# Performance work log

Measured on AMD Instinct MI355X. Metric: run time of the kernel, lower is better.

Reference implementation:

```python
import jax, jax.numpy as jnp
import numpy as np

N_NODES = 131072       # 64 graphs * 2048 nodes
N_EDGES = 2097152      # avg degree 16
N_GRAPHS = 64
NODES_PER_GRAPH = 2048
D_IN = 128
D_EMB = 64
D_HID = 128
N_ACT = 2048


def setup_inputs() -> dict:
    key = jax.random.key(0)
    ks = jax.random.split(key, 12)
    s = lambda d: 1.0 / np.sqrt(d)
    return {
        "x": jax.random.normal(ks[0], (N_NODES, D_IN), dtype=jnp.float32),
        "edge_index": jax.random.randint(ks[1], (2, N_EDGES), 0, N_NODES, dtype=jnp.int32),
        "W1l": jax.random.normal(ks[2], (D_EMB, D_IN), dtype=jnp.float32) * s(D_IN),
        "b1l": jnp.zeros((D_EMB,), dtype=jnp.float32),
        "W1r": jax.random.normal(ks[3], (D_EMB, D_IN), dtype=jnp.float32) * s(D_IN),
        "W2l": jax.random.normal(ks[4], (D_EMB, D_EMB), dtype=jnp.float32) * s(D_EMB),
        "b2l": jnp.zeros((D_EMB,), dtype=jnp.float32),
        "W2r": jax.random.normal(ks[5], (D_EMB, D_EMB), dtype=jnp.float32) * s(D_EMB),
        "fc1_W": jax.random.normal(ks[6], (D_HID, D_EMB), dtype=jnp.float32) * s(D_EMB),
        "fc1_b": jnp.zeros((D_HID,), dtype=jnp.float32),
        "fc2_W": jax.random.normal(ks[7], (N_ACT, D_HID), dtype=jnp.float32) * s(D_HID),
        "fc2_b": jnp.zeros((N_ACT,), dtype=jnp.float32),
    }


def _sage_conv(x, src, dst, Wl, bl, Wr):
    # PyG SAGEConv (mean aggr): out = lin_l(mean_{j in N(i)} x_j) + lin_r(x_i)
    msg = x[src]                                              # [E, D] gather
    agg = jax.ops.segment_sum(msg, dst, num_segments=N_NODES)  # [N, D]
    cnt = jax.ops.segment_sum(jnp.ones((src.shape[0],), x.dtype), dst,
                              num_segments=N_NODES)
    mean = agg / jnp.maximum(cnt, 1.0)[:, None]
    return mean @ Wl.T + bl + x @ Wr.T


def reference(x, edge_index, W1l, b1l, W1r, W2l, b2l, W2r,
              fc1_W, fc1_b, fc2_W, fc2_b):
    src, dst = edge_index[0], edge_index[1]
    h1 = _sage_conv(x, src, dst, W1l, b1l, W1r)    # [N, D_EMB]
    h2 = _sage_conv(h1, src, dst, W2l, b2l, W2r)   # [N, D_EMB]
    g = h2.reshape(N_GRAPHS, NODES_PER_GRAPH, D_EMB).mean(axis=1)  # [B, D_EMB]
    h = jax.nn.relu(g @ fc1_W.T + fc1_b)
    q_values = h @ fc2_W.T + fc2_b                 # [B, N_ACT]
    return q_values
```

## Files before the change

kernel.cpp:

```cpp
#include <hip/hip_runtime.h>
#include <hip/hip_bf16.h>

#define D_IN 128
#define D_EMB 64

typedef float f32x2 __attribute__((ext_vector_type(2)));
typedef float f32x4v __attribute__((ext_vector_type(4)));
typedef short bf16x8 __attribute__((ext_vector_type(8)));

static __device__ __forceinline__ unsigned short f2bf(float f) {
  __hip_bfloat16 h = __float2bfloat16(f);
  return *(unsigned short*)&h;
}

__global__ __launch_bounds__(256) void wprep_mfma_k(const float* __restrict__ W,
                                                    unsigned short* __restrict__ out,
                                                    int K) {
  int tid = blockIdx.x * 256 + threadIdx.x;
  int total = (K / 32) * 4 * 64;
  if (tid >= total) return;
  int lane = tid & 63;
  int ct = (tid >> 6) & 3;
  int s = tid >> 8;
  int row = ct * 16 + (lane & 15);
  int kk = s * 32 + (lane >> 4) * 8;
  unsigned short tmp[8];
#pragma unroll
  for (int j = 0; j < 8; j++) tmp[j] = f2bf(W[row * K + kk + j]);
  *(uint4*)&out[(size_t)tid * 8] = *(uint4*)tmp;
}


__global__ __launch_bounds__(256) void bhist1_k(const int* __restrict__ key,
                                                int* __restrict__ bh, int E) {
  __shared__ int h[256];
  const int t = threadIdx.x;
  h[t] = 0;
  __syncthreads();
  const int base = blockIdx.x * 2048;
#pragma unroll
  for (int j = 0; j < 8; j++) {
    int e = base + j * 256 + t;
    if (e < E) atomicAdd(&h[key[e] >> 9], 1);
  }
  __syncthreads();
  bh[t * 1024 + blockIdx.x] = h[t];
}

__global__ __launch_bounds__(256) void scanA_k(int* __restrict__ bh,
                                               int* __restrict__ bintot) {
  __shared__ int sa[256], sb[256];
  const int t = threadIdx.x;
  int* row = bh + (size_t)blockIdx.x * 1024;
  int v0 = row[t * 4], v1 = row[t * 4 + 1], v2 = row[t * 4 + 2], v3 = row[t * 4 + 3];
  int sum = v0 + v1 + v2 + v3;
  sa[t] = sum;
  __syncthreads();
  int* in = sa;
  int* out = sb;
  for (int st = 1; st < 256; st <<= 1) {
    out[t] = in[t] + (t >= st ? in[t - st] : 0);
    __syncthreads();
    int* tmp = in; in = out; out = tmp;
  }
  int excl = in[t] - sum;
  row[t * 4] = excl;
  row[t * 4 + 1] = excl + v0;
  row[t * 4 + 2] = excl + v0 + v1;
  row[t * 4 + 3] = excl + v0 + v1 + v2;
  if (t == 255) bintot[blockIdx.x] = in[255];
}

__global__ __launch_bounds__(256) void scanB_k(const int* __restrict__ bintot,
                                               int* __restrict__ base) {
  __shared__ int sa[256], sb[256];
  const int t = threadIdx.x;
  int v = bintot[t];
  sa[t] = v;
  __syncthreads();
  int* in = sa;
  int* out = sb;
  for (int st = 1; st < 256; st <<= 1) {
    out[t] = in[t] + (t >= st ? in[t - st] : 0);
    __syncthreads();
    int* tmp = in; in = out; out = tmp;
  }
  base[t] = in[t] - v;
  if (t == 255) base[256] = in[255];
}

__global__ __launch_bounds__(256) void sfill_k(const int* __restrict__ src,
                                               const int* __restrict__ dst,
                                               const int* __restrict__ sh,
                                               const int* __restrict__ ssub,
                                               int* __restrict__ srcS,
                                               int* __restrict__ dstS, int E) {
  __shared__ int hA[256], hB[256], runCur[256], gb[256];
  __shared__ int scache[2048];
  __shared__ int dcache[2048];
  __shared__ int sortS[2048];
  __shared__ int sortD[2048];
  __shared__ unsigned short subb[2048];
  const int t = threadIdx.x;
  const int base = blockIdx.x * 2048;
  const int n = min(2048, E - base);
  hA[t] = 0;
  __syncthreads();
#pragma unroll
  for (int j = 0; j < 8; j++) {
    int idx = j * 256 + t;
    int e = base + idx;
    if (idx < n) {
      int s = src[e];
      scache[idx] = s;
      dcache[idx] = dst[e];
      atomicAdd(&hA[s >> 9], 1);
    }
  }
  __syncthreads();
  int cnt = hA[t];
  int* in = hA;
  int* out = hB;
  for (int st = 1; st < 256; st <<= 1) {
    out[t] = in[t] + (t >= st ? in[t - st] : 0);
    __syncthreads();
    int* tmp = in; in = out; out = tmp;
  }
  int rs = in[t] - cnt;
  __syncthreads();
  hB[t] = rs;
  runCur[t] = rs;
  gb[t] = ssub[t] + sh[t * 1024 + blockIdx.x];
  __syncthreads();
#pragma unroll
  for (int j = 0; j < 8; j++) {
    int idx = j * 256 + t;
    if (idx < n) {
      int s = scache[idx];
      int b = s >> 9;
      int lpos = atomicAdd(&runCur[b], 1);
      sortS[lpos] = s;
      sortD[lpos] = dcache[idx];
      subb[lpos] = (unsigned short)b;
    }
  }
  __syncthreads();
  for (int idx = t; idx < n; idx += 256) {
    int b = subb[idx];
    int g = gb[b] + idx - hB[b];
    srcS[g] = sortS[idx];
    dstS[g] = sortD[idx];
  }
}

__global__ __launch_bounds__(256) void bfill1_k(const int* __restrict__ src,
                                                const int* __restrict__ dst,
                                                const int* __restrict__ bh,
                                                const int* __restrict__ sbase,
                                                unsigned int* __restrict__ bkt,
                                                int E) {
  __shared__ int hA[256], hB[256], runCur[256], gb[256];
  __shared__ int dcache[2048];
  __shared__ unsigned int sorted[2048];
  __shared__ unsigned short subb[2048];
  const int t = threadIdx.x;
  const int base = blockIdx.x * 2048;
  const int n = min(2048, E - base);
  hA[t] = 0;
  __syncthreads();
#pragma unroll
  for (int j = 0; j < 8; j++) {
    int idx = j * 256 + t;
    int e = base + idx;
    if (idx < n) {
      int d = dst[e];
      dcache[idx] = d;
      atomicAdd(&hA[d >> 9], 1);
    }
  }
  __syncthreads();
  int cnt = hA[t];
  int* in = hA;
  int* out = hB;
  for (int st = 1; st < 256; st <<= 1) {
    out[t] = in[t] + (t >= st ? in[t - st] : 0);
    __syncthreads();
    int* tmp = in; in = out; out = tmp;
  }
  int rs = in[t] - cnt;
  __syncthreads();
  hB[t] = rs;
  runCur[t] = rs;
  gb[t] = sbase[t] + bh[t * 1024 + blockIdx.x];
  __syncthreads();
#pragma unroll
  for (int j = 0; j < 8; j++) {
    int idx = j * 256 + t;
    int e = base + idx;
    if (idx < n) {
      int d = dcache[idx];
      int b = d >> 9;
      int lpos = atomicAdd(&runCur[b], 1);
      sorted[lpos] = ((unsigned)(d & 511) << 17) | (unsigned)src[e];
      subb[lpos] = (unsigned short)b;
    }
  }
  __syncthreads();
  for (int idx = t; idx < n; idx += 256) {
    int b = subb[idx];
    bkt[gb[b] + idx - hB[b]] = sorted[idx];
  }
}

__global__ __launch_bounds__(256) void deg4_k(const unsigned int* __restrict__ bkt,
                                              const int* __restrict__ sbase,
                                              int* __restrict__ deg) {
  __shared__ int h[512];
  const int t = threadIdx.x;
  h[t] = 0;
  h[t + 256] = 0;
  __syncthreads();
  const int i = blockIdx.x;
  const int lo = sbase[i], hi = sbase[i + 1];
  for (int e = lo + t; e < hi; e += 256) atomicAdd(&h[bkt[e] >> 17], 1);
  __syncthreads();
  deg[i * 512 + t] = h[t];
  deg[i * 512 + t + 256] = h[t + 256];
}

__global__ __launch_bounds__(256) void blocksum_k(const int* __restrict__ deg,
                                                  int* __restrict__ bsum) {
  __shared__ int sm[256];
  int t = threadIdx.x;
  sm[t] = deg[blockIdx.x * 256 + t];
  __syncthreads();
  for (int s = 128; s > 0; s >>= 1) {
    if (t < s) sm[t] += sm[t + s];
    __syncthreads();
  }
  if (t == 0) bsum[blockIdx.x] = sm[0];
}

__global__ __launch_bounds__(256) void scanbsum_k(int* __restrict__ bsum) {
  __shared__ int a[512], b[512];
  int t = threadIdx.x;
  a[t] = bsum[t];
  a[t + 256] = bsum[t + 256];
  __syncthreads();
  int* in = a;
  int* out = b;
  for (int st = 1; st < 512; st <<= 1) {
    for (int i = t; i < 512; i += 256) out[i] = in[i] + (i >= st ? in[i - st] : 0);
    __syncthreads();
    int* tmp = in; in = out; out = tmp;
  }
  for (int i = t; i < 512; i += 256) bsum[i] = (i == 0) ? 0 : in[i - 1];
}

__global__ __launch_bounds__(256) void rowptr_k(const int* __restrict__ deg,
                                                const int* __restrict__ bsumEx,
                                                int* __restrict__ rowPtr,
                                                float* __restrict__ invdeg) {
  __shared__ int a[256], b[256];
  int t = threadIdx.x;
  int i = blockIdx.x * 256 + t;
  int d = deg[i];
  a[t] = d;
  __syncthreads();
  int* in = a;
  int* out = b;
  for (int st = 1; st < 256; st <<= 1) {
    out[t] = in[t] + (t >= st ? in[t - st] : 0);
    __syncthreads();
    int* tmp = in; in = out; out = tmp;
  }
  int incl = in[t] + bsumEx[blockIdx.x];
  rowPtr[i + 1] = incl;
  invdeg[i] = 1.0f / fmaxf((float)d, 1.0f);
  if (i == 0) rowPtr[0] = 0;
}

#define CSR_CAP 12032
__global__ __launch_bounds__(256) void scat4_k(const unsigned int* __restrict__ bkt,
                                               const int* __restrict__ sbase,
                                               const int* __restrict__ rowPtr,
                                               int* __restrict__ csr) {
  __shared__ int cur[512];
  __shared__ int cbuf[CSR_CAP];
  const int t = threadIdx.x;
  const int i = blockIdx.x;
  const int node0 = i * 512;
  const int base0 = rowPtr[node0];
  cur[t] = rowPtr[node0 + t] - base0;
  cur[t + 256] = rowPtr[node0 + t + 256] - base0;
  __syncthreads();
  const int lo = sbase[i], hi = sbase[i + 1];
  for (int e = lo + t; e < hi; e += 256) {
    unsigned v = bkt[e];
    int pos = atomicAdd(&cur[v >> 17], 1);
    int sval = (int)(v & 0x1FFFFu);
    if (pos < CSR_CAP) cbuf[pos] = sval;
    else csr[base0 + pos] = sval;
  }
  __syncthreads();
  const int cnt = rowPtr[node0 + 512] - base0;
  const int lim = cnt < CSR_CAP ? cnt : CSR_CAP;
  for (int idx = t; idx < lim; idx += 256) csr[base0 + idx] = cbuf[idx];
}

template <int K, int DUAL, int ABF16>
__global__ __launch_bounds__(256) void gemm_mfma_k(const float4* __restrict__ x4,
                                                   const unsigned short* __restrict__ xb,
                                                   const unsigned short* __restrict__ wb1,
                                                   const unsigned short* __restrict__ wb2,
                                                   const float* __restrict__ bias2,
                                                   unsigned char* __restrict__ out1,
                                                   float* __restrict__ out2) {
  constexpr int K4 = K / 4;
  const int t = threadIdx.x;
  const int lane = t & 63;
  const int wv = t >> 6;
  const int col = lane & 15;
  const int quad = lane >> 4;
  const int nb = blockIdx.x * 64;
  const int arow = nb + wv * 16 + col;
  f32x4v acc1[4], acc2[4];
#pragma unroll
  for (int ct = 0; ct < 4; ct++) {
    acc1[ct] = (f32x4v){0.f, 0.f, 0.f, 0.f};
    if (DUAL) {
      float bj = bias2[ct * 16 + col];
      acc2[ct] = (f32x4v){bj, bj, bj, bj};
    }
  }
#pragma unroll
  for (int s = 0; s < K / 32; s++) {
    bf16x8 a;
    if (ABF16) {
      a = *(const bf16x8*)&xb[(size_t)arow * K + s * 32 + quad * 8];
    } else {
      float4 f0 = x4[(size_t)arow * K4 + s * 8 + quad * 2];
      float4 f1 = x4[(size_t)arow * K4 + s * 8 + quad * 2 + 1];
      unsigned short h[8];
      h[0] = f2bf(f0.x); h[1] = f2bf(f0.y); h[2] = f2bf(f0.z); h[3] = f2bf(f0.w);
      h[4] = f2bf(f1.x); h[5] = f2bf(f1.y); h[6] = f2bf(f1.z); h[7] = f2bf(f1.w);
      a = *(const bf16x8*)h;
    }
#pragma unroll
    for (int ct = 0; ct < 4; ct++) {
      bf16x8 b1 = *(const bf16x8*)&wb1[(size_t)((s * 4 + ct) * 64 + lane) * 8];
      acc1[ct] = __builtin_amdgcn_mfma_f32_16x16x32_bf16(a, b1, acc1[ct], 0, 0, 0);
      if (DUAL) {
        bf16x8 b2 = *(const bf16x8*)&wb2[(size_t)((s * 4 + ct) * 64 + lane) * 8];
        acc2[ct] = __builtin_amdgcn_mfma_f32_16x16x32_bf16(a, b2, acc2[ct], 0, 0, 0);
      }
    }
  }
#pragma unroll
  for (int ct = 0; ct < 4; ct++) {
#pragma unroll
    for (int reg = 0; reg < 4; reg++) {
      int node = nb + wv * 16 + quad * 4 + reg;
      unsigned pk = (unsigned)__builtin_amdgcn_cvt_pk_fp8_f32(acc1[ct][reg],
                                                              acc1[ct][reg], 0, false);
      out1[(size_t)node * 64 + ct * 16 + col] = (unsigned char)(pk & 0xff);
      if (DUAL) out2[(size_t)node * 64 + ct * 16 + col] = acc2[ct][reg];
    }
  }
}

template <int WRITE_H>
__global__ __launch_bounds__(256) void gather_k(const uint4* __restrict__ yb,
                                                const int* __restrict__ csr,
                                                const int* __restrict__ rowPtr,
                                                const float* __restrict__ invdeg,
                                                const float4* __restrict__ xr,
                                                unsigned short* __restrict__ hout,
                                                float* __restrict__ pm) {
  __shared__ float sg[4][4][16];
  const int t = threadIdx.x;
  const int lane = t & 63;
  const int wv = t >> 6;
  const int q = lane & 3;
  const int nl = lane >> 2;
  const int nb = blockIdx.x * 64;
  const int n = nb + wv * 16 + nl;
  const int rp0 = rowPtr[n], rp1 = rowPtr[n + 1];
  float acc[16];
#pragma unroll
  for (int k = 0; k < 16; k++) acc[k] = 0.f;
  for (int e = rp0; e < rp1; e++) {
    int s = csr[e];
    uint4 v = yb[(size_t)s * 4 + q];
    f32x2 p;
    p = __builtin_amdgcn_cvt_pk_f32_fp8(v.x, false); acc[0] += p.x;  acc[1] += p.y;
    p = __builtin_amdgcn_cvt_pk_f32_fp8(v.x, true);  acc[2] += p.x;  acc[3] += p.y;
    p = __builtin_amdgcn_cvt_pk_f32_fp8(v.y, false); acc[4] += p.x;  acc[5] += p.y;
    p = __builtin_amdgcn_cvt_pk_f32_fp8(v.y, true);  acc[6] += p.x;  acc[7] += p.y;
    p = __builtin_amdgcn_cvt_pk_f32_fp8(v.z, false); acc[8] += p.x;  acc[9] += p.y;
    p = __builtin_amdgcn_cvt_pk_f32_fp8(v.z, true);  acc[10] += p.x; acc[11] += p.y;
    p = __builtin_amdgcn_cvt_pk_f32_fp8(v.w, false); acc[12] += p.x; acc[13] += p.y;
    p = __builtin_amdgcn_cvt_pk_f32_fp8(v.w, true);  acc[14] += p.x; acc[15] += p.y;
  }
  const float sc = invdeg[n];
  float gacc[16];
  if (WRITE_H) {
    unsigned short hh[16];
#pragma unroll
    for (int u = 0; u < 4; u++) {
      float4 o = xr[(size_t)n * 16 + q * 4 + u];
      float v0 = acc[4 * u + 0] * sc + o.x;
      float v1 = acc[4 * u + 1] * sc + o.y;
      float v2 = acc[4 * u + 2] * sc + o.z;
      float v3 = acc[4 * u + 3] * sc + o.w;
      gacc[4 * u + 0] = v0; gacc[4 * u + 1] = v1;
      gacc[4 * u + 2] = v2; gacc[4 * u + 3] = v3;
      hh[4 * u + 0] = f2bf(v0); hh[4 * u + 1] = f2bf(v1);
      hh[4 * u + 2] = f2bf(v2); hh[4 * u + 3] = f2bf(v3);
    }
    *(uint4*)&hout[(size_t)n * 64 + q * 16] = *(uint4*)&hh[0];
    *(uint4*)&hout[(size_t)n * 64 + q * 16 + 8] = *(uint4*)&hh[8];
  } else {
#pragma unroll
    for (int k = 0; k < 16; k++) gacc[k] = acc[k] * sc;
  }
#pragma unroll
  for (int m = 4; m <= 32; m <<= 1)
#pragma unroll
    for (int k = 0; k < 16; k++) gacc[k] += __shfl_xor(gacc[k], m, 64);
  if (nl == 0) {
#pragma unroll
    for (int k = 0; k < 16; k++) sg[wv][q][k] = gacc[k];
  }
  __syncthreads();
  if (t < 64) {
    int qq = t >> 4, k = t & 15;
    float tot = sg[0][qq][k] + sg[1][qq][k] + sg[2][qq][k] + sg[3][qq][k];
    pm[((size_t)(blockIdx.x >> 5) * 32 + (blockIdx.x & 31)) * 64 + t] = tot;
  }
}

__global__ __launch_bounds__(256) void reduce_part_k(const float* __restrict__ pm,
                                                     float* __restrict__ gm) {
  int idx = blockIdx.x * 256 + threadIdx.x;
  int b = idx >> 6, j = idx & 63;
  float acc = 0.0f;
  for (int blk = 0; blk < 32; blk++) acc += pm[((size_t)b * 32 + blk) * 64 + j];
  gm[idx] = acc * (1.0f / 2048.0f);
}

__global__ __launch_bounds__(256) void combine_k(const float* __restrict__ gmean2,
                                                 const float* __restrict__ gmean1,
                                                 const float* __restrict__ b2l,
                                                 const float* __restrict__ W2r,
                                                 float* __restrict__ g) {
  int idx = blockIdx.x * 256 + threadIdx.x;
  int b = idx >> 6, j = idx & 63;
  const float4* m4 = (const float4*)(gmean1 + b * 64);
  const float4* w4 = (const float4*)(W2r + j * 64);
  float acc = gmean2[idx] + b2l[j];
#pragma unroll
  for (int k4 = 0; k4 < 16; k4++) {
    float4 mv = m4[k4], wv = w4[k4];
    acc += mv.x * wv.x + mv.y * wv.y + mv.z * wv.z + mv.w * wv.w;
  }
  g[idx] = acc;
}

__global__ __launch_bounds__(256) void mlp1_k(const float* __restrict__ g,
                                              const float* __restrict__ fc1_W,
                                              const float* __restrict__ fc1_b,
                                              float* __restrict__ h) {
  int idx = blockIdx.x * 256 + threadIdx.x;
  int b = idx >> 7, k = idx & 127;
  const float4* g4 = (const float4*)(g + b * 64);
  const float4* w4 = (const float4*)(fc1_W + k * 64);
  float acc = fc1_b[k];
#pragma unroll
  for (int j4 = 0; j4 < 16; j4++) {
    float4 gv = g4[j4], wv = w4[j4];
    acc += gv.x * wv.x + gv.y * wv.y + gv.z * wv.z + gv.w * wv.w;
  }
  h[idx] = fmaxf(acc, 0.0f);
}

__global__ __launch_bounds__(256) void mlp2_k(const float* __restrict__ h,
                                              const float* __restrict__ fc2_W,
                                              const float* __restrict__ fc2_b,
                                              float* __restrict__ out) {
  __shared__ float4 sh[32];
  int b = blockIdx.x >> 3;
  int a = (blockIdx.x & 7) * 256 + threadIdx.x;
  if (threadIdx.x < 32) sh[threadIdx.x] = ((const float4*)(h + b * 128))[threadIdx.x];
  __syncthreads();
  const float4* w4 = (const float4*)(fc2_W + (size_t)a * 128);
  float acc = fc2_b[a];
#pragma unroll
  for (int k4 = 0; k4 < 32; k4++) {
    float4 hv = sh[k4], wv = w4[k4];
    acc += hv.x * wv.x + hv.y * wv.y + hv.z * wv.z + hv.w * wv.w;
  }
  out[b * 2048 + a] = acc;
}

extern "C" void kernel_launch(void* const* d_in, const int* in_sizes, int n_in,
                              void* d_out, int out_size, void* d_ws, size_t ws_size,
                              hipStream_t stream) {
  const float* x     = (const float*)d_in[0];
  const int*   ei    = (const int*)d_in[1];
  const float* W1l   = (const float*)d_in[2];
  const float* b1l   = (const float*)d_in[3];
  const float* W1r   = (const float*)d_in[4];
  const float* W2l   = (const float*)d_in[5];
  const float* b2l   = (const float*)d_in[6];
  const float* W2r   = (const float*)d_in[7];
  const float* fc1_W = (const float*)d_in[8];
  const float* fc1_b = (const float*)d_in[9];
  const float* fc2_W = (const float*)d_in[10];
  const float* fc2_b = (const float*)d_in[11];
  float* out = (float*)d_out;

  const int N = in_sizes[0] / D_IN;
  const int E = in_sizes[1] / 2;
  const int* src = ei;
  const int* dst = ei + E;

  char* ws = (char*)d_ws;
  int*   deg    = (int*)ws;     ws += (size_t)N * 4;
  int*   rowPtr = (int*)ws;     ws += (size_t)(N + 256) * 4;
  int*   bsum   = (int*)ws;     ws += 512 * 4;
  float* invdeg = (float*)ws;   ws += (size_t)N * 4;
  float* gmean1 = (float*)ws;   ws += 4096 * 4;
  float* gmean2 = (float*)ws;   ws += 4096 * 4;
  float* g      = (float*)ws;   ws += 4096 * 4;
  float* hbuf   = (float*)ws;   ws += 8192 * 4;
  unsigned short* wb1l = (unsigned short*)ws;  ws += 8192 * 2;
  unsigned short* wb1r = (unsigned short*)ws;  ws += 8192 * 2;
  unsigned short* wb2l = (unsigned short*)ws;  ws += 4096 * 2;
  int*   sh     = (int*)ws;     ws += (size_t)256 * 1024 * 4;
  int*   bh     = (int*)ws;     ws += (size_t)256 * 1024 * 4;
  int*   tot    = (int*)ws;     ws += 256 * 4;
  int*   ssub   = (int*)ws;     ws += 260 * 4;
  int*   sbase  = (int*)ws;     ws += 260 * 4;
  float* p1     = (float*)ws;   ws += (size_t)64 * 32 * 64 * 4;
  float* p2     = (float*)ws;   ws += (size_t)64 * 32 * 64 * 4;
  unsigned int* bkt = (unsigned int*)ws;  ws += (size_t)E * 4;
  int*   csr    = (int*)ws;     ws += (size_t)E * 4;
  unsigned char* bufA = (unsigned char*)ws;  ws += (size_t)64 * N;
  float* bufB   = (float*)ws;   ws += (size_t)64 * N * 4;
  unsigned short* bufC = (unsigned short*)ws;  ws += (size_t)64 * N * 2;
  size_t used = (size_t)(ws - (char*)d_ws);

  int* srcS = csr;
  int* dstS = (int*)bufA;

  hipMemsetAsync(d_ws, 0, used, stream);

  wprep_mfma_k<<<4, 256, 0, stream>>>(W1l, wb1l, 128);
  wprep_mfma_k<<<4, 256, 0, stream>>>(W1r, wb1r, 128);
  wprep_mfma_k<<<2, 256, 0, stream>>>(W2l, wb2l, 64);

  const int nch = (E + 2047) >> 11;
  bhist1_k<<<nch, 256, 0, stream>>>(src, sh, E);
  scanA_k<<<256, 256, 0, stream>>>(sh, tot);
  scanB_k<<<1, 256, 0, stream>>>(tot, ssub);
  sfill_k<<<nch, 256, 0, stream>>>(src, dst, sh, ssub, srcS, dstS, E);
  bhist1_k<<<nch, 256, 0, stream>>>(dstS, bh, E);
  scanA_k<<<256, 256, 0, stream>>>(bh, tot);
  scanB_k<<<1, 256, 0, stream>>>(tot, sbase);
  bfill1_k<<<nch, 256, 0, stream>>>(srcS, dstS, bh, sbase, bkt, E);
  deg4_k<<<256, 256, 0, stream>>>(bkt, sbase, deg);
  blocksum_k<<<N / 256, 256, 0, stream>>>(deg, bsum);
  scanbsum_k<<<1, 256, 0, stream>>>(bsum);
  rowptr_k<<<N / 256, 256, 0, stream>>>(deg, bsum, rowPtr, invdeg);
  scat4_k<<<256, 256, 0, stream>>>(bkt, sbase, rowPtr, csr);

  gemm_mfma_k<128, 1, 0><<<N / 64, 256, 0, stream>>>((const float4*)x, nullptr,
                                                     wb1l, wb1r, b1l, bufA, bufB);
  gather_k<1><<<N / 64, 256, 0, stream>>>((const uint4*)bufA, csr, rowPtr, invdeg,
                                          (const float4*)bufB, bufC, p1);
  reduce_part_k<<<16, 256, 0, stream>>>(p1, gmean1);

  gemm_mfma_k<64, 0, 1><<<N / 64, 256, 0, stream>>>(nullptr, bufC, wb2l, nullptr,
                                                    nullptr, bufA, nullptr);
  gather_k<0><<<N / 64, 256, 0, stream>>>((const uint4*)bufA, csr, rowPtr, invdeg,
                                          nullptr, nullptr, p2);
  reduce_part_k<<<16, 256, 0, stream>>>(p2, gmean2);

  combine_k<<<16, 256, 0, stream>>>(gmean2, gmean1, b2l, W2r, g);
  mlp1_k<<<32, 256, 0, stream>>>(g, fc1_W, fc1_b, hbuf);
  mlp2_k<<<512, 256, 0, stream>>>(hbuf, fc2_W, fc2_b, out);
}
```

Before: 354.5 us.

## Fuse second-layer projection GEMM into first gather kernel via LDS-staged h1

The layer-1 gather kernel now keeps its bf16 h1 tile in shared memory and immediately runs the W2l MFMA projection, writing fp8 y2 directly. This drops the separate layer-2 GEMM launch and the global round trip of the bf16 h1 buffer (128 B per node written and re-read). A separate output buffer (bufD) is used so layer-1 inputs aren't overwritten while other blocks still gather from bufA. In exchange the gather kernel uses more LDS and registers, which may lower occupancy for a latency-bound gather.

```diff
diff --git a/kernel.cpp b/kernel.cpp
--- a/kernel.cpp
+++ b/kernel.cpp
@@ -308,15 +308,13 @@
   for (int idx = t; idx < lim; idx += 256) csr[base0 + idx] = cbuf[idx];
 }
 
-template <int K, int DUAL, int ABF16>
-__global__ __launch_bounds__(256) void gemm_mfma_k(const float4* __restrict__ x4,
-                                                   const unsigned short* __restrict__ xb,
-                                                   const unsigned short* __restrict__ wb1,
-                                                   const unsigned short* __restrict__ wb2,
-                                                   const float* __restrict__ bias2,
-                                                   unsigned char* __restrict__ out1,
-                                                   float* __restrict__ out2) {
-  constexpr int K4 = K / 4;
+__global__ __launch_bounds__(256) void gemm1_k(const float4* __restrict__ x4,
+                                               const unsigned short* __restrict__ wb1,
+                                               const unsigned short* __restrict__ wb2,
+                                               const float* __restrict__ bias2,
+                                               unsigned char* __restrict__ out1,
+                                               float* __restrict__ out2) {
+  constexpr int K = 128, K4 = K / 4;
   const int t = threadIdx.x;
   const int lane = t & 63;
   const int wv = t >> 6;
@@ -328,32 +326,23 @@
 #pragma unroll
   for (int ct = 0; ct < 4; ct++) {
     acc1[ct] = (f32x4v){0.f, 0.f, 0.f, 0.f};
-    if (DUAL) {
-      float bj = bias2[ct * 16 + col];
-      acc2[ct] = (f32x4v){bj, bj, bj, bj};
-    }
+    float bj = bias2[ct * 16 + col];
+    acc2[ct] = (f32x4v){bj, bj, bj, bj};
   }
 #pragma unroll
   for (int s = 0; s < K / 32; s++) {
-    bf16x8 a;
-    if (ABF16) {
-      a = *(const bf16x8*)&xb[(size_t)arow * K + s * 32 + quad * 8];
-    } else {
-      float4 f0 = x4[(size_t)arow * K4 + s * 8 + quad * 2];
-      float4 f1 = x4[(size_t)arow * K4 + s * 8 + quad * 2 + 1];
-      unsigned short h[8];
-      h[0] = f2bf(f0.x); h[1] = f2bf(f0.y); h[2] = f2bf(f0.z); h[3] = f2bf(f0.w);
-      h[4] = f2bf(f1.x); h[5] = f2bf(f1.y); h[6] = f2bf(f1.z); h[7] = f2bf(f1.w);
-      a = *(const bf16x8*)h;
-    }
+    float4 f0 = x4[(size_t)arow * K4 + s * 8 + quad * 2];
+    float4 f1 = x4[(size_t)arow * K4 + s * 8 + quad * 2 + 1];
+    unsigned short h[8];
+    h[0] = f2bf(f0.x); h[1] = f2bf(f0.y); h[2] = f2bf(f0.z); h[3] = f2bf(f0.w);
+    h[4] = f2bf(f1.x); h[5] = f2bf(f1.y); h[6] = f2bf(f1.z); h[7] = f2bf(f1.w);
+    bf16x8 a = *(const bf16x8*)h;
 #pragma unroll
     for (int ct = 0; ct < 4; ct++) {
       bf16x8 b1 = *(const bf16x8*)&wb1[(size_t)((s * 4 + ct) * 64 + lane) * 8];
       acc1[ct] = __builtin_amdgcn_mfma_f32_16x16x32_bf16(a, b1, acc1[ct], 0, 0, 0);
-      if (DUAL) {
-        bf16x8 b2 = *(const bf16x8*)&wb2[(size_t)((s * 4 + ct) * 64 + lane) * 8];
-        acc2[ct] = __builtin_amdgcn_mfma_f32_16x16x32_bf16(a, b2, acc2[ct], 0, 0, 0);
-      }
+      bf16x8 b2 = *(const bf16x8*)&wb2[(size_t)((s * 4 + ct) * 64 + lane) * 8];
+      acc2[ct] = __builtin_amdgcn_mfma_f32_16x16x32_bf16(a, b2, acc2[ct], 0, 0, 0);
     }
   }
 #pragma unroll
@@ -364,20 +353,23 @@
       unsigned pk = (unsigned)__builtin_amdgcn_cvt_pk_fp8_f32(acc1[ct][reg],
                                                               acc1[ct][reg], 0, false);
       out1[(size_t)node * 64 + ct * 16 + col] = (unsigned char)(pk & 0xff);
-      if (DUAL) out2[(size_t)node * 64 + ct * 16 + col] = acc2[ct][reg];
-    }
-  }
-}
-
-template <int WRITE_H>
+      out2[(size_t)node * 64 + ct * 16 + col] = acc2[ct][reg];
+    }
+  }
+}
+
+#define LROW 72
+template <int MODE>
 __global__ __launch_bounds__(256) void gather_k(const uint4* __restrict__ yb,
                                                 const int* __restrict__ csr,
                                                 const int* __restrict__ rowPtr,
                                                 const float* __restrict__ invdeg,
                                                 const float4* __restrict__ xr,
-                                                unsigned short* __restrict__ hout,
+                                                const unsigned short* __restrict__ wb2,
+                                                unsigned char* __restrict__ y2,
                                                 float* __restrict__ pm) {
   __shared__ float sg[4][4][16];
+  __shared__ unsigned short sh1[64 * LROW];
   const int t = threadIdx.x;
   const int lane = t & 63;
   const int wv = t >> 6;
@@ -404,7 +396,8 @@
   }
   const float sc = invdeg[n];
   float gacc[16];
-  if (WRITE_H) {
+  if (MODE) {
+    const int nloc = wv * 16 + nl;
     unsigned short hh[16];
 #pragma unroll
     for (int u = 0; u < 4; u++) {
@@ -418,8 +411,8 @@
       hh[4 * u + 0] = f2bf(v0); hh[4 * u + 1] = f2bf(v1);
       hh[4 * u + 2] = f2bf(v2); hh[4 * u + 3] = f2bf(v3);
     }
-    *(uint4*)&hout[(size_t)n * 64 + q * 16] = *(uint4*)&hh[0];
-    *(uint4*)&hout[(size_t)n * 64 + q * 16 + 8] = *(uint4*)&hh[8];
+    *(uint4*)&sh1[nloc * LROW + q * 16] = *(uint4*)&hh[0];
+    *(uint4*)&sh1[nloc * LROW + q * 16 + 8] = *(uint4*)&hh[8];
   } else {
 #pragma unroll
     for (int k = 0; k < 16; k++) gacc[k] = acc[k] * sc;
@@ -437,6 +430,32 @@
     int qq = t >> 4, k = t & 15;
     float tot = sg[0][qq][k] + sg[1][qq][k] + sg[2][qq][k] + sg[3][qq][k];
     pm[((size_t)(blockIdx.x >> 5) * 32 + (blockIdx.x & 31)) * 64 + t] = tot;
+  }
+  if (MODE) {
+    const int col = lane & 15;
+    const int quad = lane >> 4;
+    f32x4v a2[4];
+#pragma unroll
+    for (int ct = 0; ct < 4; ct++) a2[ct] = (f32x4v){0.f, 0.f, 0.f, 0.f};
+#pragma unroll
+    for (int s = 0; s < 2; s++) {
+      bf16x8 a = *(const bf16x8*)&sh1[(wv * 16 + col) * LROW + s * 32 + quad * 8];
+#pragma unroll
+      for (int ct = 0; ct < 4; ct++) {
+        bf16x8 b = *(const bf16x8*)&wb2[(size_t)((s * 4 + ct) * 64 + lane) * 8];
+        a2[ct] = __builtin_amdgcn_mfma_f32_16x16x32_bf16(a, b, a2[ct], 0, 0, 0);
+      }
+    }
+#pragma unroll
+    for (int ct = 0; ct < 4; ct++) {
+#pragma unroll
+      for (int reg = 0; reg < 4; reg++) {
+        int node = nb + wv * 16 + quad * 4 + reg;
+        unsigned pk = (unsigned)__builtin_amdgcn_cvt_pk_fp8_f32(a2[ct][reg],
+                                                                a2[ct][reg], 0, false);
+        y2[(size_t)node * 64 + ct * 16 + col] = (unsigned char)(pk & 0xff);
+      }
+    }
   }
 }
 
@@ -547,8 +566,8 @@
   unsigned int* bkt = (unsigned int*)ws;  ws += (size_t)E * 4;
   int*   csr    = (int*)ws;     ws += (size_t)E * 4;
   unsigned char* bufA = (unsigned char*)ws;  ws += (size_t)64 * N;
+  unsigned char* bufD = (unsigned char*)ws;  ws += (size_t)64 * N;
   float* bufB   = (float*)ws;   ws += (size_t)64 * N * 4;
-  unsigned short* bufC = (unsigned short*)ws;  ws += (size_t)64 * N * 2;
   size_t used = (size_t)(ws - (char*)d_ws);
 
   int* srcS = csr;
@@ -575,16 +594,13 @@
   rowptr_k<<<N / 256, 256, 0, stream>>>(deg, bsum, rowPtr, invdeg);
   scat4_k<<<256, 256, 0, stream>>>(bkt, sbase, rowPtr, csr);
 
-  gemm_mfma_k<128, 1, 0><<<N / 64, 256, 0, stream>>>((const float4*)x, nullptr,
-                                                     wb1l, wb1r, b1l, bufA, bufB);
+  gemm1_k<<<N / 64, 256, 0, stream>>>((const float4*)x, wb1l, wb1r, b1l, bufA, bufB);
   gather_k<1><<<N / 64, 256, 0, stream>>>((const uint4*)bufA, csr, rowPtr, invdeg,
-                                          (const float4*)bufB, bufC, p1);
+                                          (const float4*)bufB, wb2l, bufD, p1);
   reduce_part_k<<<16, 256, 0, stream>>>(p1, gmean1);
 
-  gemm_mfma_k<64, 0, 1><<<N / 64, 256, 0, stream>>>(nullptr, bufC, wb2l, nullptr,
-                                                    nullptr, bufA, nullptr);
-  gather_k<0><<<N / 64, 256, 0, stream>>>((const uint4*)bufA, csr, rowPtr, invdeg,
-                                          nullptr, nullptr, p2);
+  gather_k<0><<<N / 64, 256, 0, stream>>>((const uint4*)bufD, csr, rowPtr, invdeg,
+                                          nullptr, nullptr, nullptr, p2);
   reduce_part_k<<<16, 256, 0, stream>>>(p2, gmean2);
 
   combine_k<<<16, 256, 0, stream>>>(gmean2, gmean1, b2l, W2r, g);
```

After: 356.3 us. No clear change (+0.5%).
